# Kernel tuning notes

Measured on AMD Instinct MI355X. Metric: run time of the kernel, lower is better.

Reference implementation:

```python
import jax, jax.numpy as jnp
import numpy as np
from jax import lax

D_MODEL, D_INNER, D_CONV, DT_RANK, D_STATE, SEQ_LEN = 1024, 2048, 4, 64, 16, 4096


def setup_inputs() -> dict:
    key = jax.random.key(0)
    ks = jax.random.split(key, 9)
    s = 0.02
    x = jax.random.normal(ks[0], (SEQ_LEN, D_MODEL), dtype=jnp.float32)
    W_in = jax.random.normal(ks[1], (2 * D_INNER, D_MODEL), dtype=jnp.float32) * s
    conv_w = jax.random.normal(ks[2], (D_INNER, 1, D_CONV), dtype=jnp.float32) * 0.2  # depthwise (O,I/g,K)
    conv_b = jax.random.normal(ks[3], (D_INNER,), dtype=jnp.float32) * s
    W_x = jax.random.normal(ks[4], (DT_RANK + 2 * D_STATE, D_INNER), dtype=jnp.float32) * s
    W_dt = jax.random.normal(ks[5], (D_INNER, DT_RANK), dtype=jnp.float32) * s
    b_dt = jax.random.normal(ks[6], (D_INNER,), dtype=jnp.float32) * s
    # canonical S4D-real init: A[d, n] = n+1 -> A_log = log(1..d_state), tiled over d_inner
    A_log = jnp.log(jnp.tile(jnp.arange(1, D_STATE + 1, dtype=jnp.float32), (D_INNER, 1)))
    D = jnp.ones((D_INNER,), dtype=jnp.float32)
    W_out = jax.random.normal(ks[7], (D_MODEL, D_INNER), dtype=jnp.float32) * s
    return {"x": x, "W_in": W_in, "conv_w": conv_w, "conv_b": conv_b,
            "W_x": W_x, "W_dt": W_dt, "b_dt": b_dt, "A_log": A_log, "D": D,
            "W_out": W_out}


def _causal_depthwise_conv(x_ld, conv_w, conv_b):
    # x_ld: (L, d_inner). eqx Conv1d with padding=d_conv-1 then [:, :L] == left-pad causal conv.
    k = conv_w.shape[-1]
    xp = jnp.pad(x_ld, ((k - 1, 0), (0, 0)))  # (L+k-1, d)
    lhs = xp.T[None]  # (1, d, L+k-1)
    out = lax.conv_general_dilated(
        lhs, conv_w, window_strides=(1,), padding='VALID',
        dimension_numbers=('NCH', 'OIH', 'NCH'),
        feature_group_count=x_ld.shape[1])  # (1, d, L)
    return (out[0] + conv_b[:, None]).T  # (L, d)


def reference(x, W_in, conv_w, conv_b, W_x, W_dt, b_dt, A_log, D, W_out):
    L = x.shape[0]
    d_inner, d_state = A_log.shape
    dt_rank = W_dt.shape[1]

    xr = x @ W_in.T                      # (L, 2*d_inner)
    xi, res = jnp.split(xr, 2, axis=-1)  # each (L, d_inner)
    xs = jax.nn.silu(_causal_depthwise_conv(xi, conv_w, conv_b))  # (L, d_inner)

    # selective SSM
    dbl = xs @ W_x.T                     # (L, dt_rank + 2*d_state)
    dt_in, B, C = jnp.split(dbl, [dt_rank, dt_rank + d_state], axis=-1)
    delta = jax.nn.softplus(dt_in @ W_dt.T + b_dt)       # (L, d_inner)
    A = -jnp.exp(A_log)                                  # (d_inner, d_state)
    dA = jnp.exp(delta[:, :, None] * A[None])            # (L, d, n)
    dBu = delta[:, :, None] * B[:, None, :] * xs[:, :, None]  # (L, d, n)

    def step(h, ab):
        a, b = ab
        h = a * h + b
        return h, h

    _, hs = lax.scan(step, jnp.zeros((d_inner, d_state), dtype=x.dtype), (dA, dBu))
    y = jnp.einsum('ldn,ln->ld', hs, C) + xs * D         # (L, d_inner)

    y = y * jax.nn.silu(res)
    return y @ W_out.T                                   # (L, d_model)
```

## Files before the change

### kernel.cpp

```cpp
#include <hip/hip_runtime.h>
#include <cstdint>
#include <cstddef>

#define LSEQ 4096
#define DM 1024
#define DI 2048
#define DCONV 4
#define DRNK 64
#define DSTATE 16
#define DXW 96
#define NCH 64
#define CLEN 64
#define KSPLIT 8

typedef unsigned short ushort_t;
typedef __bf16 bfx8 __attribute__((ext_vector_type(8)));
typedef float  fx4  __attribute__((ext_vector_type(4)));
typedef float  fx16 __attribute__((ext_vector_type(16)));
typedef ushort_t usx8 __attribute__((ext_vector_type(8)));

__device__ __forceinline__ float siluf(float x) { return x / (1.f + __expf(-x)); }
__device__ __forceinline__ float softplusf(float x) {
  return fmaxf(x, 0.f) + log1pf(__expf(-fabsf(x)));
}
__device__ __forceinline__ ushort_t f2b(float x) {
  __bf16 b = (__bf16)x;
  return __builtin_bit_cast(ushort_t, b);
}
__device__ __forceinline__ float b2f(ushort_t u) {
  unsigned int x = ((unsigned int)u) << 16;
  return __builtin_bit_cast(float, x);
}
__device__ __forceinline__ void async16(const void* g, void* l) {
  __builtin_amdgcn_global_load_lds(
      (const __attribute__((address_space(1))) unsigned int*)g,
      (__attribute__((address_space(3))) unsigned int*)l, 16, 0, 0);
}

template <int EPI, int BN>
__global__ __launch_bounds__(256) void gemm32(
    const ushort_t* __restrict__ A, int lda,
    const ushort_t* __restrict__ B, int ldb,
    void* __restrict__ Cv, int ldc, int K)
{
  constexpr int MI = 2;
  constexpr int NJ = BN / 64;
  __shared__ ushort_t As[128 * 64];
  __shared__ ushort_t Bs[BN * 64];
  const int tid  = threadIdx.x;
  const int m0   = blockIdx.y * 128, n0 = blockIdx.x * BN;
  const int lane = tid & 63;
  const int wave = tid >> 6;
  const int wm   = (wave >> 1) * 64, wn = (wave & 1) * (BN / 2);
  const int lm   = lane & 31;
  const int kg   = lane >> 5;
  const int r0  = tid >> 3;
  const int pos = tid & 7;
  const int cswz = (pos ^ (r0 & 7)) * 8;
  const int key  = lm & 7;

  fx16 acc[MI][NJ] = {};

  const ushort_t* ga = A + (size_t)(m0 + r0) * lda + cswz;
  const ushort_t* gb = B + (size_t)(n0 + r0) * ldb + cswz;

  for (int k0 = 0; k0 < K; k0 += 64) {
#pragma unroll
    for (int t = 0; t < 4; ++t)
      async16(ga + (size_t)(32 * t) * lda + k0, &As[t * 32 * 64 + tid * 8]);
#pragma unroll
    for (int t = 0; t < BN / 32; ++t)
      async16(gb + (size_t)(32 * t) * ldb + k0, &Bs[t * 32 * 64 + tid * 8]);
    __syncthreads();

#pragma unroll
    for (int kk = 0; kk < 4; ++kk) {
      const int swz = ((kk * 2 + kg) ^ key) * 8;
      bfx8 af[MI], bfr[NJ];
#pragma unroll
      for (int i = 0; i < MI; ++i)
        af[i] = *(const bfx8*)&As[(wm + i * 32 + lm) * 64 + swz];
#pragma unroll
      for (int j = 0; j < NJ; ++j)
        bfr[j] = *(const bfx8*)&Bs[(wn + j * 32 + lm) * 64 + swz];
#pragma unroll
      for (int i = 0; i < MI; ++i)
#pragma unroll
        for (int j = 0; j < NJ; ++j)
          acc[i][j] = __builtin_amdgcn_mfma_f32_32x32x16_bf16(af[i], bfr[j], acc[i][j], 0, 0, 0);
    }
    __syncthreads();
  }

#pragma unroll
  for (int i = 0; i < MI; ++i)
#pragma unroll
    for (int j = 0; j < NJ; ++j)
#pragma unroll
      for (int r = 0; r < 16; ++r) {
        const int lrow = (r & 3) + 8 * (r >> 2) + 4 * kg;
        const size_t rowoff =
            (size_t)(m0 + wm + i * 32 + lrow) * ldc + n0 + wn + j * 32 + lm;
        if (EPI == 1) ((ushort_t*)Cv)[rowoff] = f2b(acc[i][j][r]);
        else          ((float*)Cv)[rowoff]   = acc[i][j][r];
      }
}

template <int EPI, int BN>
__global__ __launch_bounds__(256) void gemm_bf16(
    const ushort_t* __restrict__ A, int lda,
    const ushort_t* __restrict__ B, int ldb,
    void* __restrict__ Cv, int ldc, int K,
    const float* __restrict__ bias)
{
  constexpr int NJ = BN / 32;
  __shared__ ushort_t As[128 * 32];
  __shared__ ushort_t Bs[BN * 32];
  const int tid  = threadIdx.x;
  const int m0   = blockIdx.y * 128, n0 = blockIdx.x * BN;
  const int lane = tid & 63;
  const int wave = tid >> 6;
  const int wm   = (wave >> 1) * 64, wn = (wave & 1) * (BN / 2);
  const int lm   = lane & 15;
  const int r0 = tid >> 2;
  const int cswz = (((tid & 3) ^ ((r0 >> 1) & 3))) * 8;
  const int swz = (((lane >> 4) ^ ((lm >> 1) & 3))) * 8;

  fx4 acc[4][NJ] = {};

  const ushort_t* ga = A + (size_t)(m0 + r0) * lda + cswz;
  const ushort_t* gb = B + (size_t)(n0 + r0) * ldb + cswz;
  ushort_t* la0 = &As[r0 * 32 + (tid & 3) * 8];
  ushort_t* la1 = &As[(r0 + 64) * 32 + (tid & 3) * 8];
  ushort_t* lb0 = &Bs[r0 * 32 + (tid & 3) * 8];
  ushort_t* lb1 = (BN == 128) ? &Bs[(r0 + 64) * 32 + (tid & 3) * 8] : nullptr;

  for (int k0 = 0; k0 < K; k0 += 32) {
    async16(ga + k0, la0);
    async16(ga + (size_t)64 * lda + k0, la1);
    async16(gb + k0, lb0);
    if (BN == 128) async16(gb + (size_t)64 * ldb + k0, lb1);
    __syncthreads();

    bfx8 af[4], bfr[NJ];
#pragma unroll
    for (int i = 0; i < 4; ++i)
      af[i] = *(const bfx8*)&As[(wm + i * 16 + lm) * 32 + swz];
#pragma unroll
    for (int j = 0; j < NJ; ++j)
      bfr[j] = *(const bfx8*)&Bs[(wn + j * 16 + lm) * 32 + swz];
#pragma unroll
    for (int i = 0; i < 4; ++i)
#pragma unroll
      for (int j = 0; j < NJ; ++j)
        acc[i][j] = __builtin_amdgcn_mfma_f32_16x16x32_bf16(af[i], bfr[j], acc[i][j], 0, 0, 0);
    __syncthreads();
  }

  const int crow = (lane >> 4) * 4;
  const int ccol = lane & 15;
#pragma unroll
  for (int i = 0; i < 4; ++i)
#pragma unroll
    for (int r = 0; r < 4; ++r) {
      const size_t rowoff = (size_t)(m0 + wm + i * 16 + crow + r) * ldc + n0 + wn + ccol;
      if (EPI == 1) {
        ushort_t* cp = (ushort_t*)Cv + rowoff;
#pragma unroll
        for (int j = 0; j < NJ; ++j) cp[j * 16] = f2b(acc[i][j][r]);
      } else if (EPI == 2) {
        ushort_t* cp = (ushort_t*)Cv + rowoff;
        const int nb = n0 + wn + ccol;
#pragma unroll
        for (int j = 0; j < NJ; ++j)
          cp[j * 16] = f2b(softplusf(acc[i][j][r] + bias[nb + j * 16]));
      } else {
        float* cp = (float*)Cv + rowoff;
#pragma unroll
        for (int j = 0; j < NJ; ++j) cp[j * 16] = acc[i][j][r];
      }
    }
}

__global__ __launch_bounds__(256) void gemm_dbl(
    const ushort_t* __restrict__ A, const ushort_t* __restrict__ B,
    float* __restrict__ P)
{
  __shared__ ushort_t As[128 * 32];
  __shared__ ushort_t Bs[128 * 32];
  const int tid  = threadIdx.x;
  const int m0   = blockIdx.y * 128;
  const int lane = tid & 63;
  const int wave = tid >> 6;
  const int wm   = (wave >> 1) * 64, wn = (wave & 1) * 48;
  const int lm   = lane & 15;
  const int r0 = tid >> 2;
  const int cswz = (((tid & 3) ^ ((r0 >> 1) & 3))) * 8;
  const int swz  = (((lane >> 4) ^ ((lm >> 1) & 3))) * 8;
  const int kbeg = blockIdx.z * (DI / KSPLIT);

  fx4 acc[4][3] = {};

  const int brow1 = (r0 + 64 < DXW) ? r0 + 64 : DXW - 1;
  const ushort_t* ga  = A + (size_t)(m0 + r0) * DI + kbeg + cswz;
  const ushort_t* gb0 = B + (size_t)r0 * DI + kbeg + cswz;
  const ushort_t* gb1 = B + (size_t)brow1 * DI + kbeg + cswz;
  ushort_t* la0 = &As[r0 * 32 + (tid & 3) * 8];
  ushort_t* la1 = &As[(r0 + 64) * 32 + (tid & 3) * 8];
  ushort_t* lb0 = &Bs[r0 * 32 + (tid & 3) * 8];
  ushort_t* lb1 = &Bs[(r0 + 64) * 32 + (tid & 3) * 8];

  for (int k0 = 0; k0 < DI / KSPLIT; k0 += 32) {
    async16(ga + k0, la0);
    async16(ga + (size_t)64 * DI + k0, la1);
    async16(gb0 + k0, lb0);
    async16(gb1 + k0, lb1);
    __syncthreads();

    bfx8 af[4], bfr[3];
#pragma unroll
    for (int i = 0; i < 4; ++i)
      af[i] = *(const bfx8*)&As[(wm + i * 16 + lm) * 32 + swz];
#pragma unroll
    for (int j = 0; j < 3; ++j)
      bfr[j] = *(const bfx8*)&Bs[(wn + j * 16 + lm) * 32 + swz];
#pragma unroll
    for (int i = 0; i < 4; ++i)
#pragma unroll
      for (int j = 0; j < 3; ++j)
        acc[i][j] = __builtin_amdgcn_mfma_f32_16x16x32_bf16(af[i], bfr[j], acc[i][j], 0, 0, 0);
    __syncthreads();
  }

  float* base = P + (size_t)blockIdx.z * LSEQ * DXW;
  const int crow = (lane >> 4) * 4;
  const int ccol = lane & 15;
#pragma unroll
  for (int i = 0; i < 4; ++i)
#pragma unroll
    for (int r = 0; r < 4; ++r) {
      float* cp = base + (size_t)(m0 + wm + i * 16 + crow + r) * DXW + wn + ccol;
#pragma unroll
      for (int j = 0; j < 3; ++j)
        cp[j * 16] = acc[i][j][r];
    }
}

__global__ __launch_bounds__(256) void reduce_dbl(
    const float* __restrict__ P, ushort_t* __restrict__ dtb,
    float* __restrict__ dblBC)
{
  const int f = blockIdx.x * 256 + threadIdx.x;
  float s = 0.f;
#pragma unroll
  for (int z = 0; z < KSPLIT; ++z) s += P[(size_t)z * LSEQ * DXW + f];
  const int l = f / DXW;
  const int c = f - l * DXW;
  if (c < DRNK) dtb[(size_t)l * DRNK + c] = f2b(s);
  else          dblBC[(size_t)l * 32 + (c - DRNK)] = s;
}

#define CSZ0 (LSEQ * DM)
#define CSZ1 (2 * DI * DM)
#define CSZ2 (DM * DI)
#define CSZ3 (DXW * DI)
#define CSZ4 (DI * DRNK)
#define CTOT (CSZ0 + CSZ1 + CSZ2 + CSZ3 + CSZ4)

__global__ __launch_bounds__(256) void cast_all(
    const float* __restrict__ x, const float* __restrict__ W_in,
    const float* __restrict__ W_out, const float* __restrict__ W_x,
    const float* __restrict__ W_dt,
    ushort_t* __restrict__ xb, ushort_t* __restrict__ W_inb,
    ushort_t* __restrict__ W_outb, ushort_t* __restrict__ W_xb,
    ushort_t* __restrict__ W_dtb)
{
  int i = (blockIdx.x * 256 + threadIdx.x) * 4;
  if (i >= CTOT) return;
  const float* src; ushort_t* dst;
  if (i < CSZ0) { src = x + i; dst = xb + i; }
  else if (i < CSZ0 + CSZ1) { int o = i - CSZ0; src = W_in + o; dst = W_inb + o; }
  else if (i < CSZ0 + CSZ1 + CSZ2) { int o = i - CSZ0 - CSZ1; src = W_out + o; dst = W_outb + o; }
  else if (i < CSZ0 + CSZ1 + CSZ2 + CSZ3) { int o = i - CSZ0 - CSZ1 - CSZ2; src = W_x + o; dst = W_xb + o; }
  else { int o = i - CSZ0 - CSZ1 - CSZ2 - CSZ3; src = W_dt + o; dst = W_dtb + o; }
  float4 v = *(const float4*)src;
  ushort4 o4;
  o4.x = f2b(v.x); o4.y = f2b(v.y); o4.z = f2b(v.z); o4.w = f2b(v.w);
  *(ushort4*)dst = o4;
}

__global__ __launch_bounds__(256) void conv2(
    const ushort_t* __restrict__ xrb, const float* __restrict__ cw,
    const float* __restrict__ cb, ushort_t* __restrict__ xsb)
{
  const int d0 = threadIdx.x * 8;
  const int l0 = blockIdx.x * 8;

  float4 w[8];
#pragma unroll
  for (int j = 0; j < 8; ++j) w[j] = *(const float4*)(cw + (size_t)(d0 + j) * DCONV);
  float cbv[8];
  *(float4*)&cbv[0] = *(const float4*)(cb + d0);
  *(float4*)&cbv[4] = *(const float4*)(cb + d0 + 4);

  float h0[8], h1[8], h2[8];
#pragma unroll
  for (int j = 0; j < 8; ++j) { h0[j] = 0.f; h1[j] = 0.f; h2[j] = 0.f; }
  if (l0 >= 3) {
    usx8 u0 = *(const usx8*)(xrb + (size_t)(l0 - 3) * (2 * DI) + d0);
    usx8 u1 = *(const usx8*)(xrb + (size_t)(l0 - 2) * (2 * DI) + d0);
    usx8 u2 = *(const usx8*)(xrb + (size_t)(l0 - 1) * (2 * DI) + d0);
#pragma unroll
    for (int j = 0; j < 8; ++j) { h0[j] = b2f(u0[j]); h1[j] = b2f(u1[j]); h2[j] = b2f(u2[j]); }
  }

#pragma unroll
  for (int i = 0; i < 8; ++i) {
    const int l = l0 + i;
    usx8 uc = *(const usx8*)(xrb + (size_t)l * (2 * DI) + d0);
    float c[8];
#pragma unroll
    for (int j = 0; j < 8; ++j) c[j] = b2f(uc[j]);
    usx8 o;
#pragma unroll
    for (int j = 0; j < 8; ++j) {
      float acc = cbv[j];
      acc = fmaf(w[j].x, h0[j], acc);
      acc = fmaf(w[j].y, h1[j], acc);
      acc = fmaf(w[j].z, h2[j], acc);
      acc = fmaf(w[j].w, c[j], acc);
      o[j] = f2b(siluf(acc));
    }
    *(usx8*)(xsb + (size_t)l * DI + d0) = o;
#pragma unroll
    for (int j = 0; j < 8; ++j) { h0[j] = h1[j]; h1[j] = h2[j]; h2[j] = c[j]; }
  }
}

__device__ __forceinline__ bool chain_ok(const float* Av) {
  bool ok = true;
#pragma unroll
  for (int n = 0; n < DSTATE; ++n)
    ok = ok && (fabsf(Av[n] + (float)(n + 1)) < 1e-4f);
  return ok;
}

__global__ __launch_bounds__(256) void scan_pass1(
    const ushort_t* __restrict__ deltab, const ushort_t* __restrict__ xsb,
    const float* __restrict__ dblBC, const float* __restrict__ A_log,
    float* __restrict__ cP, float* __restrict__ cS)
{
  const int tid = threadIdx.x;
  const int g = blockIdx.x;
  const int c = blockIdx.y;
  const int d = g * 256 + tid;
  __shared__ ushort_t Dsh[CLEN * 256];
  __shared__ ushort_t Ush[CLEN * 256];
  __shared__ float Bsh[CLEN][DSTATE];

  const size_t rowbase = (size_t)(c * CLEN) * DI + g * 256;
  for (int i = tid; i < CLEN * 32; i += 256) {
    const int l = i >> 5;
    const int o = (i & 31) * 8;
    *(usx8*)&Dsh[l * 256 + o] = *(const usx8*)(deltab + rowbase + (size_t)l * DI + o);
    *(usx8*)&Ush[l * 256 + o] = *(const usx8*)(xsb   + rowbase + (size_t)l * DI + o);
  }
  for (int i = tid; i < CLEN * DSTATE; i += 256) {
    const int l = i >> 4, n = i & 15;
    Bsh[l][n] = dblBC[(size_t)(c * CLEN + l) * 32 + n];
  }
  __syncthreads();

  float Av[DSTATE], h[DSTATE];
#pragma unroll
  for (int n = 0; n < DSTATE; ++n) {
    Av[n] = -__expf(A_log[d * DSTATE + n]);
    h[n] = 0.f;
  }
  const size_t base = (size_t)c * DI * DSTATE + (size_t)d * DSTATE;

  if (chain_ok(Av)) {
    float sd = 0.f;
    for (int l = 0; l < CLEN; ++l) {
      const float dlt = b2f(Dsh[l * 256 + tid]);
      const float du = dlt * b2f(Ush[l * 256 + tid]);
      sd += dlt;
      const float q = __expf(-dlt);
      float dAn = 1.f;
#pragma unroll
      for (int n = 0; n < DSTATE; ++n) {
        dAn *= q;
        h[n] = fmaf(dAn, h[n], du * Bsh[l][n]);
      }
    }
    const float Qc = __expf(-sd);
    float Pn = 1.f;
#pragma unroll
    for (int n = 0; n < DSTATE; ++n) {
      Pn *= Qc;
      cP[base + n] = Pn; cS[base + n] = h[n];
    }
  } else {
    float P[DSTATE];
#pragma unroll
    for (int n = 0; n < DSTATE; ++n) P[n] = 1.f;
    for (int l = 0; l < CLEN; ++l) {
      const float dlt = b2f(Dsh[l * 256 + tid]);
      const float du = dlt * b2f(Ush[l * 256 + tid]);
#pragma unroll
      for (int n = 0; n < DSTATE; ++n) {
        const float dA = __expf(dlt * Av[n]);
        h[n] = fmaf(dA, h[n], du * Bsh[l][n]);
        P[n] *= dA;
      }
    }
#pragma unroll
    for (int n = 0; n < DSTATE; ++n) { cP[base + n] = P[n]; cS[base + n] = h[n]; }
  }
}

__global__ __launch_bounds__(256) void scan_pass2(
    const float* __restrict__ cP, const float* __restrict__ cS,
    float* __restrict__ ch0)
{
  const int dn = blockIdx.x * 256 + threadIdx.x;
  float h = 0.f;
  for (int c = 0; c < NCH; ++c) {
    const size_t o = (size_t)c * DI * DSTATE + dn;
    const float p = cP[o], s = cS[o];
    ch0[o] = h;
    h = fmaf(p, h, s);
  }
}

__global__ __launch_bounds__(256) void scan_pass3(
    const ushort_t* __restrict__ deltab, const ushort_t* __restrict__ xsb,
    const float* __restrict__ dblBC, const float* __restrict__ A_log,
    const float* __restrict__ ch0, const float* __restrict__ Dp,
    const ushort_t* __restrict__ xrb, ushort_t* __restrict__ y1b)
{
  const int tid = threadIdx.x;
  const int g = blockIdx.x;
  const int c = blockIdx.y;
  const int d = g * 256 + tid;
  __shared__ ushort_t Dsh[CLEN * 256];
  __shared__ ushort_t Ush[CLEN * 256];
  __shared__ float Bsh[CLEN][DSTATE];
  __shared__ float Csh[CLEN][DSTATE];

  const size_t rowbase = (size_t)(c * CLEN) * DI + g * 256;
  for (int i = tid; i < CLEN * 32; i += 256) {
    const int l = i >> 5;
    const int o = (i & 31) * 8;
    *(usx8*)&Dsh[l * 256 + o] = *(const usx8*)(deltab + rowbase + (size_t)l * DI + o);
    *(usx8*)&Ush[l * 256 + o] = *(const usx8*)(xsb   + rowbase + (size_t)l * DI + o);
  }
  for (int i = tid; i < CLEN * DSTATE; i += 256) {
    const int l = i >> 4, n = i & 15;
    const size_t row = (size_t)(c * CLEN + l) * 32;
    Bsh[l][n] = dblBC[row + n];
    Csh[l][n] = dblBC[row + 16 + n];
  }
  __syncthreads();

  float Av[DSTATE], h[DSTATE];
  const size_t base = (size_t)c * DI * DSTATE + (size_t)d * DSTATE;
#pragma unroll
  for (int n = 0; n < DSTATE; ++n) {
    Av[n] = -__expf(A_log[d * DSTATE + n]);
    h[n] = ch0[base + n];
  }
  const float Dd = Dp[d];
  const ushort_t* resp = xrb + (size_t)(c * CLEN) * (2 * DI) + DI + d;
  ushort_t* yp = y1b + (size_t)(c * CLEN) * DI + d;

  if (chain_ok(Av)) {
    for (int l = 0; l < CLEN; ++l) {
      const float dlt = b2f(Dsh[l * 256 + tid]);
      const float u = b2f(Ush[l * 256 + tid]);
      const float du = dlt * u;
      const float q = __expf(-dlt);
      float dAn = 1.f;
      float y = 0.f;
#pragma unroll
      for (int n = 0; n < DSTATE; ++n) {
        dAn *= q;
        h[n] = fmaf(dAn, h[n], du * Bsh[l][n]);
        y = fmaf(h[n], Csh[l][n], y);
      }
      y = fmaf(u, Dd, y);
      const float res = b2f(resp[(size_t)l * (2 * DI)]);
      yp[(size_t)l * DI] = f2b(y * siluf(res));
    }
  } else {
    for (int l = 0; l < CLEN; ++l) {
      const float dlt = b2f(Dsh[l * 256 + tid]);
      const float u = b2f(Ush[l * 256 + tid]);
      const float du = dlt * u;
      float y = 0.f;
#pragma unroll
      for (int n = 0; n < DSTATE; ++n) {
        const float dA = __expf(dlt * Av[n]);
        h[n] = fmaf(dA, h[n], du * Bsh[l][n]);
        y = fmaf(h[n], Csh[l][n], y);
      }
      y = fmaf(u, Dd, y);
      const float res = b2f(resp[(size_t)l * (2 * DI)]);
      yp[(size_t)l * DI] = f2b(y * siluf(res));
    }
  }
}

extern "C" void kernel_launch(void* const* d_in, const int* in_sizes, int n_in,
                              void* d_out, int out_size, void* d_ws, size_t ws_size,
                              hipStream_t stream) {
  (void)in_sizes; (void)n_in; (void)out_size; (void)ws_size;
  const float* x      = (const float*)d_in[0];
  const float* W_in   = (const float*)d_in[1];
  const float* conv_w = (const float*)d_in[2];
  const float* conv_b = (const float*)d_in[3];
  const float* W_x    = (const float*)d_in[4];
  const float* W_dt   = (const float*)d_in[5];
  const float* b_dt   = (const float*)d_in[6];
  const float* A_log  = (const float*)d_in[7];
  const float* Dp     = (const float*)d_in[8];
  const float* W_out  = (const float*)d_in[9];
  float* out = (float*)d_out;

  float* ws    = (float*)d_ws;
  float* cP    = ws;
  float* cS    = cP + (size_t)NCH * DI * DSTATE;
  ushort_t* deltab = (ushort_t*)(cS + (size_t)NCH * DI * DSTATE);
  ushort_t* xrb   = deltab + (size_t)LSEQ * DI;
  ushort_t* xsb   = xrb   + (size_t)LSEQ * 2 * DI;
  ushort_t* y1b   = xsb   + (size_t)LSEQ * DI;
  ushort_t* xb    = y1b   + (size_t)LSEQ * DI;
  ushort_t* W_inb = xb    + (size_t)LSEQ * DM;
  ushort_t* W_outb= W_inb + (size_t)2 * DI * DM;
  ushort_t* W_xb  = W_outb+ (size_t)DM * DI;
  ushort_t* W_dtb = W_xb  + (size_t)DXW * DI;
  ushort_t* dtb   = W_dtb + (size_t)DI * DRNK;
  float* dblBC = (float*)(dtb + (size_t)LSEQ * DRNK);
  float* partial = cP;
  float* ch0 = cP;

  hipLaunchKernelGGL(cast_all, dim3((CTOT / 4 + 255) / 256), dim3(256), 0, stream,
                     x, W_in, W_out, W_x, W_dt, xb, W_inb, W_outb, W_xb, W_dtb);

  hipLaunchKernelGGL(HIP_KERNEL_NAME(gemm32<1, 128>),
                     dim3((2 * DI) / 128, LSEQ / 128), dim3(256), 0, stream,
                     xb, DM, W_inb, DM, (void*)xrb, 2 * DI, DM);

  hipLaunchKernelGGL(conv2, dim3(LSEQ / 8), dim3(256), 0, stream,
                     xrb, conv_w, conv_b, xsb);

  hipLaunchKernelGGL(gemm_dbl, dim3(1, LSEQ / 128, KSPLIT), dim3(256), 0, stream,
                     xsb, W_xb, partial);
  hipLaunchKernelGGL(reduce_dbl, dim3((LSEQ * DXW) / 256), dim3(256), 0, stream,
                     partial, dtb, dblBC);

  hipLaunchKernelGGL(HIP_KERNEL_NAME(gemm_bf16<2, 128>),
                     dim3(DI / 128, LSEQ / 128), dim3(256), 0, stream,
                     dtb, DRNK, W_dtb, DRNK, (void*)deltab, DI, DRNK, b_dt);

  hipLaunchKernelGGL(scan_pass1, dim3(DI / 256, NCH), dim3(256), 0, stream,
                     deltab, xsb, dblBC, A_log, cP, cS);
  hipLaunchKernelGGL(scan_pass2, dim3((DI * DSTATE) / 256), dim3(256), 0, stream,
                     cP, cS, ch0);
  hipLaunchKernelGGL(scan_pass3, dim3(DI / 256, NCH), dim3(256), 0, stream,
                     deltab, xsb, dblBC, A_log, ch0, Dp, xrb, y1b);

  hipLaunchKernelGGL(HIP_KERNEL_NAME(gemm32<0, 64>),
                     dim3(DM / 64, LSEQ / 128), dim3(256), 0, stream,
                     y1b, DI, W_outb, DI, (void*)out, DM, DI);
}
```

Before: 294.3 us.

## Specialize delta GEMM for K=64 and store chunk delta sums instead of decay products

```diff
diff --git a/kernel.cpp b/kernel.cpp
--- a/kernel.cpp
+++ b/kernel.cpp
@@ -106,78 +106,64 @@
       }
 }
 
-template <int EPI, int BN>
-__global__ __launch_bounds__(256) void gemm_bf16(
-    const ushort_t* __restrict__ A, int lda,
-    const ushort_t* __restrict__ B, int ldb,
-    void* __restrict__ Cv, int ldc, int K,
-    const float* __restrict__ bias)
-{
-  constexpr int NJ = BN / 32;
-  __shared__ ushort_t As[128 * 32];
-  __shared__ ushort_t Bs[BN * 32];
+__global__ __launch_bounds__(256) void gemm_delta(
+    const ushort_t* __restrict__ A,
+    const ushort_t* __restrict__ B,
+    const float* __restrict__ bias,
+    ushort_t* __restrict__ C)
+{
+  __shared__ ushort_t As[128 * 64];
+  __shared__ ushort_t Bs[128 * 64];
   const int tid  = threadIdx.x;
-  const int m0   = blockIdx.y * 128, n0 = blockIdx.x * BN;
+  const int m0   = blockIdx.y * 128, n0 = blockIdx.x * 128;
   const int lane = tid & 63;
   const int wave = tid >> 6;
-  const int wm   = (wave >> 1) * 64, wn = (wave & 1) * (BN / 2);
-  const int lm   = lane & 15;
-  const int r0 = tid >> 2;
-  const int cswz = (((tid & 3) ^ ((r0 >> 1) & 3))) * 8;
-  const int swz = (((lane >> 4) ^ ((lm >> 1) & 3))) * 8;
-
-  fx4 acc[4][NJ] = {};
-
-  const ushort_t* ga = A + (size_t)(m0 + r0) * lda + cswz;
-  const ushort_t* gb = B + (size_t)(n0 + r0) * ldb + cswz;
-  ushort_t* la0 = &As[r0 * 32 + (tid & 3) * 8];
-  ushort_t* la1 = &As[(r0 + 64) * 32 + (tid & 3) * 8];
-  ushort_t* lb0 = &Bs[r0 * 32 + (tid & 3) * 8];
-  ushort_t* lb1 = (BN == 128) ? &Bs[(r0 + 64) * 32 + (tid & 3) * 8] : nullptr;
-
-  for (int k0 = 0; k0 < K; k0 += 32) {
-    async16(ga + k0, la0);
-    async16(ga + (size_t)64 * lda + k0, la1);
-    async16(gb + k0, lb0);
-    if (BN == 128) async16(gb + (size_t)64 * ldb + k0, lb1);
-    __syncthreads();
-
-    bfx8 af[4], bfr[NJ];
-#pragma unroll
-    for (int i = 0; i < 4; ++i)
-      af[i] = *(const bfx8*)&As[(wm + i * 16 + lm) * 32 + swz];
-#pragma unroll
-    for (int j = 0; j < NJ; ++j)
-      bfr[j] = *(const bfx8*)&Bs[(wn + j * 16 + lm) * 32 + swz];
-#pragma unroll
-    for (int i = 0; i < 4; ++i)
-#pragma unroll
-      for (int j = 0; j < NJ; ++j)
-        acc[i][j] = __builtin_amdgcn_mfma_f32_16x16x32_bf16(af[i], bfr[j], acc[i][j], 0, 0, 0);
-    __syncthreads();
-  }
-
-  const int crow = (lane >> 4) * 4;
-  const int ccol = lane & 15;
-#pragma unroll
-  for (int i = 0; i < 4; ++i)
-#pragma unroll
-    for (int r = 0; r < 4; ++r) {
-      const size_t rowoff = (size_t)(m0 + wm + i * 16 + crow + r) * ldc + n0 + wn + ccol;
-      if (EPI == 1) {
-        ushort_t* cp = (ushort_t*)Cv + rowoff;
-#pragma unroll
-        for (int j = 0; j < NJ; ++j) cp[j * 16] = f2b(acc[i][j][r]);
-      } else if (EPI == 2) {
-        ushort_t* cp = (ushort_t*)Cv + rowoff;
-        const int nb = n0 + wn + ccol;
-#pragma unroll
-        for (int j = 0; j < NJ; ++j)
-          cp[j * 16] = f2b(softplusf(acc[i][j][r] + bias[nb + j * 16]));
-      } else {
-        float* cp = (float*)Cv + rowoff;
-#pragma unroll
-        for (int j = 0; j < NJ; ++j) cp[j * 16] = acc[i][j][r];
+  const int wm   = (wave >> 1) * 64, wn = (wave & 1) * 64;
+  const int lm   = lane & 31;
+  const int kg   = lane >> 5;
+  const int r0  = tid >> 3;
+  const int pos = tid & 7;
+  const int cswz = (pos ^ (r0 & 7)) * 8;
+  const int key  = lm & 7;
+
+  fx16 acc[2][2] = {};
+
+#pragma unroll
+  for (int t = 0; t < 4; ++t)
+    async16(A + (size_t)(m0 + r0 + 32 * t) * DRNK + cswz, &As[t * 32 * 64 + tid * 8]);
+#pragma unroll
+  for (int t = 0; t < 4; ++t)
+    async16(B + (size_t)(n0 + r0 + 32 * t) * DRNK + cswz, &Bs[t * 32 * 64 + tid * 8]);
+  __syncthreads();
+
+#pragma unroll
+  for (int kk = 0; kk < 4; ++kk) {
+    const int swz = ((kk * 2 + kg) ^ key) * 8;
+    bfx8 af[2], bfr[2];
+#pragma unroll
+    for (int i = 0; i < 2; ++i)
+      af[i] = *(const bfx8*)&As[(wm + i * 32 + lm) * 64 + swz];
+#pragma unroll
+    for (int j = 0; j < 2; ++j)
+      bfr[j] = *(const bfx8*)&Bs[(wn + j * 32 + lm) * 64 + swz];
+#pragma unroll
+    for (int i = 0; i < 2; ++i)
+#pragma unroll
+      for (int j = 0; j < 2; ++j)
+        acc[i][j] = __builtin_amdgcn_mfma_f32_32x32x16_bf16(af[i], bfr[j], acc[i][j], 0, 0, 0);
+  }
+
+#pragma unroll
+  for (int i = 0; i < 2; ++i)
+#pragma unroll
+    for (int j = 0; j < 2; ++j) {
+      const int col = n0 + wn + j * 32 + lm;
+      const float bv = bias[col];
+#pragma unroll
+      for (int r = 0; r < 16; ++r) {
+        const int lrow = (r & 3) + 8 * (r >> 2) + 4 * kg;
+        C[(size_t)(m0 + wm + i * 32 + lrow) * DI + col] =
+            f2b(softplusf(acc[i][j][r] + bv));
       }
     }
 }
@@ -348,7 +334,7 @@
 __global__ __launch_bounds__(256) void scan_pass1(
     const ushort_t* __restrict__ deltab, const ushort_t* __restrict__ xsb,
     const float* __restrict__ dblBC, const float* __restrict__ A_log,
-    float* __restrict__ cP, float* __restrict__ cS)
+    float* __restrict__ sd, float* __restrict__ cS)
 {
   const int tid = threadIdx.x;
   const int g = blockIdx.x;
@@ -378,13 +364,13 @@
     h[n] = 0.f;
   }
   const size_t base = (size_t)c * DI * DSTATE + (size_t)d * DSTATE;
+  float sdv = 0.f;
 
   if (chain_ok(Av)) {
-    float sd = 0.f;
     for (int l = 0; l < CLEN; ++l) {
       const float dlt = b2f(Dsh[l * 256 + tid]);
       const float du = dlt * b2f(Ush[l * 256 + tid]);
-      sd += dlt;
+      sdv += dlt;
       const float q = __expf(-dlt);
       float dAn = 1.f;
 #pragma unroll
@@ -393,41 +379,35 @@
         h[n] = fmaf(dAn, h[n], du * Bsh[l][n]);
       }
     }
-    const float Qc = __expf(-sd);
-    float Pn = 1.f;
-#pragma unroll
-    for (int n = 0; n < DSTATE; ++n) {
-      Pn *= Qc;
-      cP[base + n] = Pn; cS[base + n] = h[n];
-    }
   } else {
-    float P[DSTATE];
-#pragma unroll
-    for (int n = 0; n < DSTATE; ++n) P[n] = 1.f;
     for (int l = 0; l < CLEN; ++l) {
       const float dlt = b2f(Dsh[l * 256 + tid]);
       const float du = dlt * b2f(Ush[l * 256 + tid]);
+      sdv += dlt;
 #pragma unroll
       for (int n = 0; n < DSTATE; ++n) {
         const float dA = __expf(dlt * Av[n]);
         h[n] = fmaf(dA, h[n], du * Bsh[l][n]);
-        P[n] *= dA;
       }
     }
-#pragma unroll
-    for (int n = 0; n < DSTATE; ++n) { cP[base + n] = P[n]; cS[base + n] = h[n]; }
-  }
-}
-
-__global__ __launch_bounds__(256) void scan_pass2(
-    const float* __restrict__ cP, const float* __restrict__ cS,
-    float* __restrict__ ch0)
-{
-  const int dn = blockIdx.x * 256 + threadIdx.x;
+  }
+  sd[(size_t)c * DI + d] = sdv;
+#pragma unroll
+  for (int n = 0; n < DSTATE; ++n) cS[base + n] = h[n];
+}
+
+__global__ __launch_bounds__(64) void scan_pass2(
+    const float* __restrict__ sd, const float* __restrict__ cS,
+    const float* __restrict__ A_log, float* __restrict__ ch0)
+{
+  const int dn = blockIdx.x * 64 + threadIdx.x;
+  const int d = dn >> 4;
+  const float av = -__expf(A_log[dn]);
   float h = 0.f;
   for (int c = 0; c < NCH; ++c) {
     const size_t o = (size_t)c * DI * DSTATE + dn;
-    const float p = cP[o], s = cS[o];
+    const float s = cS[o];
+    const float p = __expf(av * sd[(size_t)c * DI + d]);
     ch0[o] = h;
     h = fmaf(p, h, s);
   }
@@ -528,9 +508,10 @@
   float* out = (float*)d_out;
 
   float* ws    = (float*)d_ws;
-  float* cP    = ws;
-  float* cS    = cP + (size_t)NCH * DI * DSTATE;
-  ushort_t* deltab = (ushort_t*)(cS + (size_t)NCH * DI * DSTATE);
+  float* sd    = ws;
+  float* cS    = sd + (size_t)NCH * DI;
+  float* ch0   = cS + (size_t)NCH * DI * DSTATE;
+  ushort_t* deltab = (ushort_t*)(ch0 + (size_t)NCH * DI * DSTATE);
   ushort_t* xrb   = deltab + (size_t)LSEQ * DI;
   ushort_t* xsb   = xrb   + (size_t)LSEQ * 2 * DI;
   ushort_t* y1b   = xsb   + (size_t)LSEQ * DI;
@@ -541,8 +522,7 @@
   ushort_t* W_dtb = W_xb  + (size_t)DXW * DI;
   ushort_t* dtb   = W_dtb + (size_t)DI * DRNK;
   float* dblBC = (float*)(dtb + (size_t)LSEQ * DRNK);
-  float* partial = cP;
-  float* ch0 = cP;
+  float* partial = ws;
 
   hipLaunchKernelGGL(cast_all, dim3((CTOT / 4 + 255) / 256), dim3(256), 0, stream,
                      x, W_in, W_out, W_x, W_dt, xb, W_inb, W_outb, W_xb, W_dtb);
@@ -559,14 +539,13 @@
   hipLaunchKernelGGL(reduce_dbl, dim3((LSEQ * DXW) / 256), dim3(256), 0, stream,
                      partial, dtb, dblBC);
 
-  hipLaunchKernelGGL(HIP_KERNEL_NAME(gemm_bf16<2, 128>),
-                     dim3(DI / 128, LSEQ / 128), dim3(256), 0, stream,
-                     dtb, DRNK, W_dtb, DRNK, (void*)deltab, DI, DRNK, b_dt);
+  hipLaunchKernelGGL(gemm_delta, dim3(DI / 128, LSEQ / 128), dim3(256), 0, stream,
+                     dtb, W_dtb, b_dt, deltab);
 
   hipLaunchKernelGGL(scan_pass1, dim3(DI / 256, NCH), dim3(256), 0, stream,
-                     deltab, xsb, dblBC, A_log, cP, cS);
-  hipLaunchKernelGGL(scan_pass2, dim3((DI * DSTATE) / 256), dim3(256), 0, stream,
-                     cP, cS, ch0);
+                     deltab, xsb, dblBC, A_log, sd, cS);
+  hipLaunchKernelGGL(scan_pass2, dim3((DI * DSTATE) / 64), dim3(64), 0, stream,
+                     sd, cS, A_log, ch0);
   hipLaunchKernelGGL(scan_pass3, dim3(DI / 256, NCH), dim3(256), 0, stream,
                      deltab, xsb, dblBC, A_log, ch0, Dp, xrb, y1b);
 
```

Result: faster. 287.9 us (-2.2%).
